# Optimization experiments

Hardware: AMD Instinct MI355X
Metric: run time of the kernel (lower is better)

## Reference

```python
import jax, jax.numpy as jnp
import numpy as np

N = 50000
E = 800000
IN_F = 128
HID = 128
CLS = 32
H = 4
K_HOPS = 2
BETA_MUL = 1.0


def _transconv(x, edge, Wq, bq, Wk, bk, Wv, bv):
    # x: [N, F_in]; edge: [2, E]; W*: [A, F_in]; b*: [A]
    n = x.shape[0]
    q = x @ Wq.T + bq
    k = x @ Wk.T + bk
    v = x @ Wv.T + bv
    A = q.shape[1]
    d_k = A // H
    q = q.reshape(n, H, d_k)
    k = k.reshape(n, H, d_k)
    v = v.reshape(n, H, d_k)
    src, dst = edge[0], edge[1]
    # per-edge dot-product scores: [E, H]
    scores = jnp.einsum('ehd,ehd->eh', q[src], k[dst]) / float(np.sqrt(d_k))
    # segment softmax over source node index (torch_geometric softmax semantics)
    m = jax.ops.segment_max(scores, src, num_segments=n)
    e = jnp.exp(scores - m[src])
    denom = jax.ops.segment_sum(e, src, num_segments=n)
    attn = e / (denom[src] + 1e-16)
    # spmm: out[src] += attn * v[dst], per head; head-major concat == reshape
    msg = attn[:, :, None] * v[dst]              # [E, H, d_k]
    out = jax.ops.segment_sum(msg, src, num_segments=n)  # [N, H, d_k]
    return out.reshape(n, H * d_k)


def _layer(feat, edges, Wq, bq, Wk, bk, Wv, bv):
    # HigherOrderGATLayer with agg_type='sum' + single head with agg_func='mean'
    out = None
    for kk in range(K_HOPS):
        beta = 1.0 if kk == 0 else BETA_MUL / (kk + 1)
        p = beta * _transconv(feat, edges[kk], Wq[kk], bq[kk], Wk[kk], bk[kk], Wv[kk], bv[kk])
        out = p if out is None else out + p
    return out


def setup_inputs() -> dict:
    key = jax.random.key(0)
    ks = jax.random.split(key, 20)
    s = 0.05
    inp = {
        'x': jax.random.normal(ks[0], (N, IN_F), dtype=jnp.float32),
        'Wq0': s * jax.random.normal(ks[1], (K_HOPS, HID, IN_F), dtype=jnp.float32),
        'bq0': s * jax.random.normal(ks[2], (K_HOPS, HID), dtype=jnp.float32),
        'Wk0': s * jax.random.normal(ks[3], (K_HOPS, HID, IN_F), dtype=jnp.float32),
        'bk0': s * jax.random.normal(ks[4], (K_HOPS, HID), dtype=jnp.float32),
        'Wv0': s * jax.random.normal(ks[5], (K_HOPS, HID, IN_F), dtype=jnp.float32),
        'bv0': s * jax.random.normal(ks[6], (K_HOPS, HID), dtype=jnp.float32),
        'Wq1': s * jax.random.normal(ks[7], (K_HOPS, CLS, HID), dtype=jnp.float32),
        'bq1': s * jax.random.normal(ks[8], (K_HOPS, CLS), dtype=jnp.float32),
        'Wk1': s * jax.random.normal(ks[9], (K_HOPS, CLS, HID), dtype=jnp.float32),
        'bk1': s * jax.random.normal(ks[10], (K_HOPS, CLS), dtype=jnp.float32),
        'Wv1': s * jax.random.normal(ks[11], (K_HOPS, CLS, HID), dtype=jnp.float32),
        'bv1': s * jax.random.normal(ks[12], (K_HOPS, CLS), dtype=jnp.float32),
        'edge_l0_k0': jax.random.randint(ks[13], (2, E), 0, N, dtype=jnp.int32).astype(jnp.int64),
        'edge_l0_k1': jax.random.randint(ks[14], (2, E), 0, N, dtype=jnp.int32).astype(jnp.int64),
        'edge_l1_k0': jax.random.randint(ks[15], (2, E), 0, N, dtype=jnp.int32).astype(jnp.int64),
        'edge_l1_k1': jax.random.randint(ks[16], (2, E), 0, N, dtype=jnp.int32).astype(jnp.int64),
    }
    return inp


def reference(x, Wq0, bq0, Wk0, bk0, Wv0, bv0, Wq1, bq1, Wk1, bk1, Wv1, bv1,
              edge_l0_k0, edge_l0_k1, edge_l1_k0, edge_l1_k1):
    edges0 = [edge_l0_k0, edge_l0_k1]
    edges1 = [edge_l1_k0, edge_l1_k1]
    h = jax.nn.elu(_layer(x, edges0, Wq0, bq0, Wk0, bk0, Wv0, bv0))
    logits = _layer(h, edges1, Wq1, bq1, Wk1, bk1, Wv1, bv1)
    return jax.nn.log_softmax(logits, axis=-1)
```

## Files before the change

### kernel.cpp

```cpp
#include <hip/hip_runtime.h>
#include <hip/hip_bf16.h>
#include <math.h>

#define N_NODES 50000
#define N_EDGES 800000
#define IN_F    128
#define HID     128
#define CLS     32
#define NHEAD   4
#define NBUCK   196

typedef __attribute__((ext_vector_type(8))) short  short8;
typedef __attribute__((ext_vector_type(4))) float  floatx4;
typedef __attribute__((ext_vector_type(2))) float  f32x2;
typedef _Float16 h2 __attribute__((ext_vector_type(2)));

static __device__ __forceinline__ unsigned short f2bf(float f) {
    unsigned int u = __float_as_uint(f);
    return (unsigned short)((u + 0x7fffu + ((u >> 16) & 1u)) >> 16);
}
static __device__ __forceinline__ unsigned short f2h(float f) {
    return __builtin_bit_cast(unsigned short, (_Float16)f);
}
static __device__ __forceinline__ h2 uh2(unsigned int u) {
    return __builtin_bit_cast(h2, u);
}
static __device__ __forceinline__ float elu1(float x) {
    return x > 0.f ? x : expm1f(x);
}

static __device__ __forceinline__ float dot8h(uint4 qw, uint4 kw) {
    h2 d = uh2(qw.x) * uh2(kw.x);
    d += uh2(qw.y) * uh2(kw.y);
    d += uh2(qw.z) * uh2(kw.z);
    d += uh2(qw.w) * uh2(kw.w);
    return (float)d.x + (float)d.y;
}

static __device__ __forceinline__ float dot8f8(const float* qf, uint2 kw) {
    f32x2 a0 = __builtin_amdgcn_cvt_pk_f32_fp8((int)kw.x, false);
    f32x2 a1 = __builtin_amdgcn_cvt_pk_f32_fp8((int)kw.x, true);
    f32x2 a2 = __builtin_amdgcn_cvt_pk_f32_fp8((int)kw.y, false);
    f32x2 a3 = __builtin_amdgcn_cvt_pk_f32_fp8((int)kw.y, true);
    return fmaf(qf[0], a0.x, fmaf(qf[1], a0.y, fmaf(qf[2], a1.x, fmaf(qf[3], a1.y,
           fmaf(qf[4], a2.x, fmaf(qf[5], a2.y, fmaf(qf[6], a3.x, qf[7] * a3.y)))))));
}
static __device__ __forceinline__ void acc8f8(float* ax, float e, uint2 vw) {
    f32x2 a0 = __builtin_amdgcn_cvt_pk_f32_fp8((int)vw.x, false);
    f32x2 a1 = __builtin_amdgcn_cvt_pk_f32_fp8((int)vw.x, true);
    f32x2 a2 = __builtin_amdgcn_cvt_pk_f32_fp8((int)vw.y, false);
    f32x2 a3 = __builtin_amdgcn_cvt_pk_f32_fp8((int)vw.y, true);
    ax[0] = fmaf(e, a0.x, ax[0]); ax[1] = fmaf(e, a0.y, ax[1]);
    ax[2] = fmaf(e, a1.x, ax[2]); ax[3] = fmaf(e, a1.y, ax[3]);
    ax[4] = fmaf(e, a2.x, ax[4]); ax[5] = fmaf(e, a2.y, ax[5]);
    ax[6] = fmaf(e, a3.x, ax[6]); ax[7] = fmaf(e, a3.y, ax[7]);
}

__global__ __launch_bounds__(256) void conv6(
    const float* __restrict__ a0, const float* __restrict__ a1, const float* __restrict__ a2,
    const float* __restrict__ a3, const float* __restrict__ a4, const float* __restrict__ a5,
    unsigned short* __restrict__ o0, unsigned short* __restrict__ o1, unsigned short* __restrict__ o2,
    unsigned short* __restrict__ o3, unsigned short* __restrict__ o4, unsigned short* __restrict__ o5,
    int cBig, int cSmall)
{
    const float* srcs[6] = {a0, a1, a2, a3, a4, a5};
    unsigned short* dsts[6] = {o0, o1, o2, o3, o4, o5};
    int s = blockIdx.y;
    int count = (s < 3) ? cBig : cSmall;
    int i = blockIdx.x * 256 + threadIdx.x;
    if (i < count) dsts[s][i] = f2bf(srcs[s][i]);
}

__global__ __launch_bounds__(256) void bucket_hist(
    const int* __restrict__ e0, const int* __restrict__ e1,
    const int* __restrict__ e2, const int* __restrict__ e3,
    int* __restrict__ bcnt, int nE)
{
    const int s = blockIdx.y;
    const int* ep = (s == 0) ? e0 : (s == 1) ? e1 : (s == 2) ? e2 : e3;
    __shared__ int h[NBUCK];
    for (int i = threadIdx.x; i < NBUCK; i += 256) h[i] = 0;
    __syncthreads();
    for (int e = blockIdx.x * 256 + threadIdx.x; e < nE; e += gridDim.x * 256)
        atomicAdd(&h[ep[e] >> 8], 1);
    __syncthreads();
    for (int i = threadIdx.x; i < NBUCK; i += 256)
        if (h[i]) atomicAdd(&bcnt[s * NBUCK + i], h[i]);
}

__global__ __launch_bounds__(256) void bucket_scan(
    const int* __restrict__ bcnt, int* __restrict__ bbase, int* __restrict__ bcur)
{
    int s = blockIdx.x;
    __shared__ int tmp[256];
    int v = (threadIdx.x < NBUCK) ? bcnt[s * NBUCK + threadIdx.x] : 0;
    tmp[threadIdx.x] = v; __syncthreads();
    for (int o = 1; o < 256; o <<= 1) {
        int t = (threadIdx.x >= o) ? tmp[threadIdx.x - o] : 0;
        __syncthreads(); tmp[threadIdx.x] += t; __syncthreads();
    }
    int excl = tmp[threadIdx.x] - v;
    if (threadIdx.x < NBUCK) {
        bbase[s * (NBUCK + 1) + threadIdx.x] = excl;
        bcur[s * NBUCK + threadIdx.x] = excl;
    }
    if (threadIdx.x == NBUCK - 1)
        bbase[s * (NBUCK + 1) + NBUCK] = excl + v;
}

#define TILE 8192
__global__ __launch_bounds__(256) void pass1_scatter(
    const int* __restrict__ e0, const int* __restrict__ e1,
    const int* __restrict__ e2, const int* __restrict__ e3,
    int* __restrict__ bcur, unsigned int* __restrict__ pairs, int nE)
{
    const int s = blockIdx.y;
    const int* ep = (s == 0) ? e0 : (s == 1) ? e1 : (s == 2) ? e2 : e3;
    const int tile0 = blockIdx.x * TILE;
    __shared__ int hist[NBUCK], base[NBUCK], cur[NBUCK];
    for (int i = threadIdx.x; i < NBUCK; i += 256) { hist[i] = 0; cur[i] = 0; }
    __syncthreads();
    for (int i = threadIdx.x; i < TILE; i += 256) {
        int e = tile0 + i;
        if (e < nE) atomicAdd(&hist[ep[e] >> 8], 1);
    }
    __syncthreads();
    for (int i = threadIdx.x; i < NBUCK; i += 256)
        base[i] = hist[i] ? atomicAdd(&bcur[s * NBUCK + i], hist[i]) : 0;
    __syncthreads();
    unsigned int* pp = pairs + (size_t)s * nE;
    for (int i = threadIdx.x; i < TILE; i += 256) {
        int e = tile0 + i;
        if (e < nE) {
            int src = ep[e], dst = ep[e + nE];
            int b = src >> 8;
            int r = atomicAdd(&cur[b], 1);
            pp[base[b] + r] = ((unsigned int)(src & 255) << 16) | (unsigned int)dst;
        }
    }
}

__global__ __launch_bounds__(256) void pass2_place(
    const unsigned int* __restrict__ pairs, const int* __restrict__ bbase,
    int* __restrict__ rowptr, int* __restrict__ deg, int* __restrict__ col,
    int nE, int n)
{
    const int s = blockIdx.y, b = blockIdx.x;
    const int base0 = bbase[s * (NBUCK + 1) + b];
    const int ecnt  = bbase[s * (NBUCK + 1) + b + 1] - base0;
    const unsigned int* pp = pairs + (size_t)s * nE + base0;
    __shared__ int hist[256], cur[256];
    hist[threadIdx.x] = 0;
    __syncthreads();
    for (int i = threadIdx.x; i < ecnt; i += 256)
        atomicAdd(&hist[(pp[i] >> 16) & 255], 1);
    __syncthreads();
    int v = hist[threadIdx.x];
    cur[threadIdx.x] = v; __syncthreads();
    for (int o = 1; o < 256; o <<= 1) {
        int t = (threadIdx.x >= o) ? cur[threadIdx.x - o] : 0;
        __syncthreads(); cur[threadIdx.x] += t; __syncthreads();
    }
    int excl = cur[threadIdx.x] - v;
    int node = b * 256 + threadIdx.x;
    if (node < n) {
        rowptr[(size_t)s * n + node] = base0 + excl;
        deg[(size_t)s * n + node] = v;
    }
    __syncthreads();
    cur[threadIdx.x] = excl;
    __syncthreads();
    int* colp = col + (size_t)s * nE + base0;
    for (int i = threadIdx.x; i < ecnt; i += 256) {
        unsigned int pr = pp[i];
        int r = atomicAdd(&cur[(pr >> 16) & 255], 1);
        colp[r] = (int)(pr & 0xffffu);
    }
}

static __device__ __forceinline__ short8 pack8(const float* p) {
    float4 a = *(const float4*)p;
    float4 b = *(const float4*)(p + 4);
    short8 v;
    v[0] = (short)f2bf(a.x); v[1] = (short)f2bf(a.y);
    v[2] = (short)f2bf(a.z); v[3] = (short)f2bf(a.w);
    v[4] = (short)f2bf(b.x); v[5] = (short)f2bf(b.y);
    v[6] = (short)f2bf(b.z); v[7] = (short)f2bf(b.w);
    return v;
}

template<int A, bool KV8>
__global__ __launch_bounds__(256) void qkv_lds(
    const float* __restrict__ x,
    const unsigned short* __restrict__ Wq, const float* __restrict__ bq,
    const unsigned short* __restrict__ Wk, const float* __restrict__ bk,
    const unsigned short* __restrict__ Wv, const float* __restrict__ bv,
    unsigned short* __restrict__ q0, unsigned short* __restrict__ q1,
    void* __restrict__ k0, void* __restrict__ k1,
    void* __restrict__ v0, void* __restrict__ v1,
    int n)
{
    constexpr int NT   = A / 16;
    constexpr int WROW = IN_F + 8;
    constexpr int OROW = A + 8;
    __shared__ unsigned short Wb[A * WROW];
    __shared__ unsigned short Ob[64 * OROW];

    const int t    = threadIdx.x;
    const int wave = t >> 6;
    const int lane = t & 63;
    const int r    = lane & 15;
    const int kg   = lane >> 4;
    const int node0 = blockIdx.x * 64;
    const int myrow = wave * 16 + r;
    const int xnode = min(node0 + myrow, n - 1);

    short8 xf[4];
    const float* xr = x + (size_t)xnode * IN_F + kg * 8;
#pragma unroll
    for (int ks = 0; ks < 4; ++ks) xf[ks] = pack8(xr + ks * 32);

    const size_t off = (size_t)A * IN_F;
    const unsigned short* Ws[6] = {Wq, Wk, Wv, Wq + off, Wk + off, Wv + off};
    const float*          bs[6] = {bq, bk, bv, bq + A, bk + A, bv + A};
    void*                 os[6] = {q0, k0, v0, q1, k1, v1};

    for (int s = 0; s < 6; ++s) {
        const unsigned short* Wg = Ws[s];
#pragma unroll
        for (int it = 0; it < A * IN_F / 2048; ++it) {
            int e = (it * 256 + t) * 8;
            int row = e / IN_F, c = e % IN_F;
            *(uint4*)&Wb[row * WROW + c] = *(const uint4*)&Wg[e];
        }
        __syncthreads();

        floatx4 acc[NT];
        const float* b = bs[s];
#pragma unroll
        for (int nt = 0; nt < NT; ++nt) {
            float4 b4 = *(const float4*)(b + nt * 16 + kg * 4);
            acc[nt] = (floatx4){b4.x, b4.y, b4.z, b4.w};
        }
#pragma unroll
        for (int ks = 0; ks < 4; ++ks) {
#pragma unroll
            for (int nt = 0; nt < NT; ++nt) {
                short8 wf = *(const short8*)&Wb[(nt * 16 + r) * WROW + ks * 32 + kg * 8];
                acc[nt] = __builtin_amdgcn_mfma_f32_16x16x32_bf16(wf, xf[ks], acc[nt], 0, 0, 0);
            }
        }

        const bool f8 = KV8 && (s != 0) && (s != 3);
        if (f8) {
            unsigned char* Obb = (unsigned char*)Ob;
#pragma unroll
            for (int nt = 0; nt < NT; ++nt) {
                int p = __builtin_amdgcn_cvt_pk_fp8_f32(acc[nt][0], acc[nt][1], 0, false);
                p     = __builtin_amdgcn_cvt_pk_fp8_f32(acc[nt][2], acc[nt][3], p, true);
                *(unsigned int*)&Obb[myrow * OROW + nt * 16 + kg * 4] = (unsigned int)p;
            }
        } else {
#pragma unroll
            for (int nt = 0; nt < NT; ++nt) {
                unsigned int lo = (unsigned int)f2h(acc[nt][0]) | ((unsigned int)f2h(acc[nt][1]) << 16);
                unsigned int hi = (unsigned int)f2h(acc[nt][2]) | ((unsigned int)f2h(acc[nt][3]) << 16);
                *(uint2*)&Ob[myrow * OROW + nt * 16 + kg * 4] = make_uint2(lo, hi);
            }
        }
        __syncthreads();

        if (f8) {
            const unsigned char* Obb = (const unsigned char*)Ob;
            unsigned char* og = (unsigned char*)os[s];
#pragma unroll
            for (int it = 0; it < 64 * A / 2048; ++it) {
                int g = (it * 256 + t) * 8;
                int row = g / A, c = g % A;
                int gn = node0 + row;
                if (gn < n)
                    *(uint2*)&og[(size_t)gn * A + c] = *(const uint2*)&Obb[row * OROW + c];
            }
        } else {
            unsigned short* og = (unsigned short*)os[s];
#pragma unroll
            for (int it = 0; it < 64 * A / 2048; ++it) {
                int g = (it * 256 + t) * 8;
                int row = g / A, c = g % A;
                int gn = node0 + row;
                if (gn < n)
                    *(uint4*)&og[(size_t)gn * A + c] = *(const uint4*)&Ob[row * OROW + c];
            }
        }
        __syncthreads();
    }
}

__device__ __forceinline__ void gat_phase128(
    const unsigned short* __restrict__ q, const uint2* __restrict__ kb,
    const uint2* __restrict__ vb,
    const int* __restrict__ rowptr, const int* __restrict__ deg,
    const int* __restrict__ col,
    int wid, int eslot, int il, float scale, float* r)
{
    uint4 qw = *(const uint4*)(q + (size_t)wid * 128 + il * 8);
    float qf[8];
    {
        h2 t0 = uh2(qw.x), t1 = uh2(qw.y), t2 = uh2(qw.z), t3 = uh2(qw.w);
        qf[0] = (float)t0.x; qf[1] = (float)t0.y;
        qf[2] = (float)t1.x; qf[3] = (float)t1.y;
        qf[4] = (float)t2.x; qf[5] = (float)t2.y;
        qf[6] = (float)t3.x; qf[7] = (float)t3.y;
    }
    int start = rowptr[wid], cnt = deg[wid];
    float l = 0.f;
    float ax[8];
#pragma unroll
    for (int j = 0; j < 8; ++j) ax[j] = 0.f;

    int t = eslot;
    for (; t + 4 < cnt; t += 8) {
        int d0 = col[start + t], d1 = col[start + t + 4];
        uint2 kw0 = kb[(size_t)d0 * 16 + il];
        uint2 kw1 = kb[(size_t)d1 * 16 + il];
        uint2 vw0 = vb[(size_t)d0 * 16 + il];
        uint2 vw1 = vb[(size_t)d1 * 16 + il];
        float p0 = dot8f8(qf, kw0);
        float p1 = dot8f8(qf, kw1);
        p0 += __shfl_xor(p0, 1); p0 += __shfl_xor(p0, 2);
        p1 += __shfl_xor(p1, 1); p1 += __shfl_xor(p1, 2);
        float e0 = __expf(p0 * scale);
        float e1 = __expf(p1 * scale);
        l += e0 + e1;
        acc8f8(ax, e0, vw0);
        acc8f8(ax, e1, vw1);
    }
    for (; t < cnt; t += 4) {
        int d = col[start + t];
        uint2 kw = kb[(size_t)d * 16 + il];
        uint2 vw = vb[(size_t)d * 16 + il];
        float p = dot8f8(qf, kw);
        p += __shfl_xor(p, 1); p += __shfl_xor(p, 2);
        float e = __expf(p * scale);
        l += e;
        acc8f8(ax, e, vw);
    }
#pragma unroll
    for (int off = 16; off <= 32; off <<= 1) {
        l += __shfl_xor(l, off);
#pragma unroll
        for (int j = 0; j < 8; ++j) ax[j] += __shfl_xor(ax[j], off);
    }
    float inv = (l > 0.f) ? 1.f / l : 0.f;
#pragma unroll
    for (int j = 0; j < 8; ++j) r[j] = ax[j] * inv;
}

__global__ __launch_bounds__(256) void gat2_128(
    const unsigned short* __restrict__ q0, const unsigned short* __restrict__ q1,
    const uint2* __restrict__ k0, const uint2* __restrict__ v0,
    const uint2* __restrict__ k1, const uint2* __restrict__ v1,
    const int* __restrict__ rp0, const int* __restrict__ dg0, const int* __restrict__ cl0,
    const int* __restrict__ rp1, const int* __restrict__ dg1, const int* __restrict__ cl1,
    float* __restrict__ out, float scale, int n)
{
    int wid  = (blockIdx.x * 256 + threadIdx.x) >> 6;
    int lane = threadIdx.x & 63;
    if (wid >= n) return;
    int eslot = lane >> 4, il = lane & 15;

    float r0[8], r1[8];
    gat_phase128(q0, k0, v0, rp0, dg0, cl0, wid, eslot, il, scale, r0);
    gat_phase128(q1, k1, v1, rp1, dg1, cl1, wid, eslot, il, scale, r1);

    if (eslot == 0) {
        float z[8];
#pragma unroll
        for (int j = 0; j < 8; ++j) z[j] = elu1(r0[j] + 0.5f * r1[j]);
        float4* op = (float4*)(out + (size_t)wid * 128 + il * 8);
        op[0] = make_float4(z[0], z[1], z[2], z[3]);
        op[1] = make_float4(z[4], z[5], z[6], z[7]);
    }
}

__device__ __forceinline__ void gat_phase32(
    const unsigned short* __restrict__ q, const uint4* __restrict__ kb,
    const uint4* __restrict__ vb,
    const int* __restrict__ rowptr, const int* __restrict__ deg,
    const int* __restrict__ col,
    int wid, int eslot, int il, float scale, float* r)
{
    uint4 qw = *(const uint4*)(q + (size_t)wid * 32 + il * 8);
    int start = rowptr[wid], cnt = deg[wid];
    float l = 0.f;
    h2 ax2[4];
#pragma unroll
    for (int j = 0; j < 4; ++j) ax2[j] = (h2){(_Float16)0.f, (_Float16)0.f};

    for (int t = eslot; t < cnt; t += 16) {
        int d = col[start + t];
        uint4 kw = kb[(size_t)d * 4 + il];
        uint4 vw = vb[(size_t)d * 4 + il];
        float p = dot8h(qw, kw);
        float e = __expf(p * scale);
        l += e;
        _Float16 h = (_Float16)e;
        h2 e2 = (h2){h, h};
        ax2[0] += e2 * uh2(vw.x); ax2[1] += e2 * uh2(vw.y);
        ax2[2] += e2 * uh2(vw.z); ax2[3] += e2 * uh2(vw.w);
    }
    float ax[8];
#pragma unroll
    for (int j = 0; j < 4; ++j) { ax[2 * j] = (float)ax2[j].x; ax[2 * j + 1] = (float)ax2[j].y; }
#pragma unroll
    for (int off = 4; off <= 32; off <<= 1) {
        l += __shfl_xor(l, off);
#pragma unroll
        for (int j = 0; j < 8; ++j) ax[j] += __shfl_xor(ax[j], off);
    }
    float inv = (l > 0.f) ? 1.f / l : 0.f;
#pragma unroll
    for (int j = 0; j < 8; ++j) r[j] = ax[j] * inv;
}

__global__ __launch_bounds__(256) void gat2_32(
    const unsigned short* __restrict__ q0, const unsigned short* __restrict__ q1,
    const uint4* __restrict__ k0, const uint4* __restrict__ v0,
    const uint4* __restrict__ k1, const uint4* __restrict__ v1,
    const int* __restrict__ rp0, const int* __restrict__ dg0, const int* __restrict__ cl0,
    const int* __restrict__ rp1, const int* __restrict__ dg1, const int* __restrict__ cl1,
    float* __restrict__ outp, float scale, int n)
{
    int wid  = (blockIdx.x * 256 + threadIdx.x) >> 6;
    int lane = threadIdx.x & 63;
    if (wid >= n) return;
    int eslot = lane >> 2, il = lane & 3;

    float r0[8], r1[8];
    gat_phase32(q0, k0, v0, rp0, dg0, cl0, wid, eslot, il, scale, r0);
    gat_phase32(q1, k1, v1, rp1, dg1, cl1, wid, eslot, il, scale, r1);

    if (eslot == 0) {
        float z[8];
#pragma unroll
        for (int j = 0; j < 8; ++j) z[j] = r0[j] + 0.5f * r1[j];
        float mx = z[0];
#pragma unroll
        for (int j = 1; j < 8; ++j) mx = fmaxf(mx, z[j]);
        mx = fmaxf(mx, __shfl_xor(mx, 1));
        mx = fmaxf(mx, __shfl_xor(mx, 2));
        float sm = 0.f;
#pragma unroll
        for (int j = 0; j < 8; ++j) sm += __expf(z[j] - mx);
        sm += __shfl_xor(sm, 1);
        sm += __shfl_xor(sm, 2);
        float lse = mx + logf(sm);
        float4* op = (float4*)(outp + (size_t)wid * 32 + il * 8);
        op[0] = make_float4(z[0] - lse, z[1] - lse, z[2] - lse, z[3] - lse);
        op[1] = make_float4(z[4] - lse, z[5] - lse, z[6] - lse, z[7] - lse);
    }
}

extern "C" void kernel_launch(void* const* d_in, const int* in_sizes, int n_in,
                              void* d_out, int out_size, void* d_ws, size_t ws_size,
                              hipStream_t stream)
{
    const float* x   = (const float*)d_in[0];
    const float* Wq0 = (const float*)d_in[1];
    const float* bq0 = (const float*)d_in[2];
    const float* Wk0 = (const float*)d_in[3];
    const float* bk0 = (const float*)d_in[4];
    const float* Wv0 = (const float*)d_in[5];
    const float* bv0 = (const float*)d_in[6];
    const float* Wq1 = (const float*)d_in[7];
    const float* bq1 = (const float*)d_in[8];
    const float* Wk1 = (const float*)d_in[9];
    const float* bk1 = (const float*)d_in[10];
    const float* Wv1 = (const float*)d_in[11];
    const float* bv1 = (const float*)d_in[12];
    const int* e0 = (const int*)d_in[13];
    const int* e1 = (const int*)d_in[14];
    const int* e2 = (const int*)d_in[15];
    const int* e3 = (const int*)d_in[16];

    char* w = (char*)d_ws;
    unsigned short* q0h = (unsigned short*)w; w += (size_t)N_NODES * HID * 2;
    unsigned short* q1h = (unsigned short*)w; w += (size_t)N_NODES * HID * 2;
    unsigned char*  k0c = (unsigned char*)w;  w += (size_t)N_NODES * HID;
    unsigned char*  v0c = (unsigned char*)w;  w += (size_t)N_NODES * HID;
    unsigned char*  k1c = (unsigned char*)w;  w += (size_t)N_NODES * HID;
    unsigned char*  v1c = (unsigned char*)w;  w += (size_t)N_NODES * HID;
    float*          acc = (float*)w;          w += (size_t)N_NODES * HID * 4;
    int* deg    = (int*)w; w += (size_t)4 * N_NODES * 4;
    int* rowptr = (int*)w; w += (size_t)4 * N_NODES * 4;
    int* col    = (int*)w; w += (size_t)4 * N_EDGES * 4;
    int* bcnt   = (int*)w; w += (size_t)4 * NBUCK * 4;
    int* bbase  = (int*)w; w += (size_t)4 * (NBUCK + 1) * 4;
    int* bcur   = (int*)w; w += (size_t)4 * NBUCK * 4;
    unsigned short* wq0b = (unsigned short*)w; w += (size_t)2 * HID * IN_F * 2;
    unsigned short* wk0b = (unsigned short*)w; w += (size_t)2 * HID * IN_F * 2;
    unsigned short* wv0b = (unsigned short*)w; w += (size_t)2 * HID * IN_F * 2;
    unsigned short* wq1b = (unsigned short*)w; w += (size_t)2 * CLS * IN_F * 2;
    unsigned short* wk1b = (unsigned short*)w; w += (size_t)2 * CLS * IN_F * 2;
    unsigned short* wv1b = (unsigned short*)w; w += (size_t)2 * CLS * IN_F * 2;

    unsigned int* pairs = (unsigned int*)q0h;
    unsigned short* qA0 = q0h;
    unsigned short* qA1 = q0h + (size_t)N_NODES * CLS;
    unsigned short* kA0 = q0h + (size_t)2 * N_NODES * CLS;
    unsigned short* vA0 = q0h + (size_t)3 * N_NODES * CLS;
    unsigned short* kA1 = q1h;
    unsigned short* vA1 = q1h + (size_t)N_NODES * CLS;

    float* out = (float*)d_out;
    const int NB = (N_NODES + 3) / 4;
    const int QB = (N_NODES + 63) / 64;
    const float sc0 = 1.f / sqrtf(32.f), sc1 = 1.f / sqrtf(8.f);

    const int W0 = 2 * HID * IN_F, W1 = 2 * CLS * IN_F;
    conv6<<<dim3((W0 + 255) / 256, 6), 256, 0, stream>>>(
        Wq0, Wk0, Wv0, Wq1, Wk1, Wv1, wq0b, wk0b, wv0b, wq1b, wk1b, wv1b, W0, W1);

    hipMemsetAsync(bcnt, 0, (size_t)4 * NBUCK * 4, stream);
    bucket_hist<<<dim3(256, 4), 256, 0, stream>>>(e0, e1, e2, e3, bcnt, N_EDGES);
    bucket_scan<<<4, 256, 0, stream>>>(bcnt, bbase, bcur);
    pass1_scatter<<<dim3((N_EDGES + TILE - 1) / TILE, 4), 256, 0, stream>>>(
        e0, e1, e2, e3, bcur, pairs, N_EDGES);
    pass2_place<<<dim3(NBUCK, 4), 256, 0, stream>>>(
        pairs, bbase, rowptr, deg, col, N_EDGES, N_NODES);

    qkv_lds<HID, true><<<QB, 256, 0, stream>>>(
        x, wq0b, bq0, wk0b, bk0, wv0b, bv0,
        q0h, q1h, k0c, k1c, v0c, v1c, N_NODES);
    gat2_128<<<NB, 256, 0, stream>>>(
        q0h, q1h,
        (const uint2*)k0c, (const uint2*)v0c, (const uint2*)k1c, (const uint2*)v1c,
        rowptr,            deg,            col,
        rowptr + N_NODES,  deg + N_NODES,  col + N_EDGES,
        acc, sc0, N_NODES);

    qkv_lds<CLS, false><<<QB, 256, 0, stream>>>(
        acc, wq1b, bq1, wk1b, bk1, wv1b, bv1,
        qA0, qA1, kA0, kA1, vA0, vA1, N_NODES);
    gat2_32<<<NB, 256, 0, stream>>>(
        qA0, qA1,
        (const uint4*)kA0, (const uint4*)vA0, (const uint4*)kA1, (const uint4*)vA1,
        rowptr + 2 * N_NODES, deg + 2 * N_NODES, col + (size_t)2 * N_EDGES,
        rowptr + 3 * N_NODES, deg + 3 * N_NODES, col + (size_t)3 * N_EDGES,
        out, sc1, N_NODES);
}
```

Baseline: 283.9 us.

## Store layer-1 keys and values in FP8 and use 32-bit gather indexing

After: 281.1 us. No clear change (-1.0%).

```diff
diff --git a/kernel.cpp b/kernel.cpp
--- a/kernel.cpp
+++ b/kernel.cpp
@@ -29,21 +29,16 @@
     return x > 0.f ? x : expm1f(x);
 }
 
-static __device__ __forceinline__ float dot8h(uint4 qw, uint4 kw) {
-    h2 d = uh2(qw.x) * uh2(kw.x);
-    d += uh2(qw.y) * uh2(kw.y);
-    d += uh2(qw.z) * uh2(kw.z);
-    d += uh2(qw.w) * uh2(kw.w);
-    return (float)d.x + (float)d.y;
-}
-
 static __device__ __forceinline__ float dot8f8(const float* qf, uint2 kw) {
     f32x2 a0 = __builtin_amdgcn_cvt_pk_f32_fp8((int)kw.x, false);
     f32x2 a1 = __builtin_amdgcn_cvt_pk_f32_fp8((int)kw.x, true);
     f32x2 a2 = __builtin_amdgcn_cvt_pk_f32_fp8((int)kw.y, false);
     f32x2 a3 = __builtin_amdgcn_cvt_pk_f32_fp8((int)kw.y, true);
-    return fmaf(qf[0], a0.x, fmaf(qf[1], a0.y, fmaf(qf[2], a1.x, fmaf(qf[3], a1.y,
-           fmaf(qf[4], a2.x, fmaf(qf[5], a2.y, fmaf(qf[6], a3.x, qf[7] * a3.y)))))));
+    float p0 = fmaf(qf[0], a0.x, qf[1] * a0.y);
+    p0 = fmaf(qf[2], a1.x, fmaf(qf[3], a1.y, p0));
+    float p1 = fmaf(qf[4], a2.x, qf[5] * a2.y);
+    p1 = fmaf(qf[6], a3.x, fmaf(qf[7], a3.y, p1));
+    return p0 + p1;
 }
 static __device__ __forceinline__ void acc8f8(float* ax, float e, uint2 vw) {
     f32x2 a0 = __builtin_amdgcn_cvt_pk_f32_fp8((int)vw.x, false);
@@ -216,7 +211,7 @@
     const int xnode = min(node0 + myrow, n - 1);
 
     short8 xf[4];
-    const float* xr = x + (size_t)xnode * IN_F + kg * 8;
+    const float* xr = x + (unsigned)xnode * IN_F + kg * 8;
 #pragma unroll
     for (int ks = 0; ks < 4; ++ks) xf[ks] = pack8(xr + ks * 32);
 
@@ -279,7 +274,7 @@
                 int row = g / A, c = g % A;
                 int gn = node0 + row;
                 if (gn < n)
-                    *(uint2*)&og[(size_t)gn * A + c] = *(const uint2*)&Obb[row * OROW + c];
+                    *(uint2*)&og[(unsigned)gn * A + c] = *(const uint2*)&Obb[row * OROW + c];
             }
         } else {
             unsigned short* og = (unsigned short*)os[s];
@@ -289,7 +284,7 @@
                 int row = g / A, c = g % A;
                 int gn = node0 + row;
                 if (gn < n)
-                    *(uint4*)&og[(size_t)gn * A + c] = *(const uint4*)&Ob[row * OROW + c];
+                    *(uint4*)&og[(unsigned)gn * A + c] = *(const uint4*)&Ob[row * OROW + c];
             }
         }
         __syncthreads();
@@ -303,7 +298,7 @@
     const int* __restrict__ col,
     int wid, int eslot, int il, float scale, float* r)
 {
-    uint4 qw = *(const uint4*)(q + (size_t)wid * 128 + il * 8);
+    uint4 qw = *(const uint4*)(q + (unsigned)wid * 128u + (unsigned)(il * 8));
     float qf[8];
     {
         h2 t0 = uh2(qw.x), t1 = uh2(qw.y), t2 = uh2(qw.z), t3 = uh2(qw.w);
@@ -320,11 +315,12 @@
 
     int t = eslot;
     for (; t + 4 < cnt; t += 8) {
-        int d0 = col[start + t], d1 = col[start + t + 4];
-        uint2 kw0 = kb[(size_t)d0 * 16 + il];
-        uint2 kw1 = kb[(size_t)d1 * 16 + il];
-        uint2 vw0 = vb[(size_t)d0 * 16 + il];
-        uint2 vw1 = vb[(size_t)d1 * 16 + il];
+        unsigned d0 = (unsigned)col[start + t] * 16u + (unsigned)il;
+        unsigned d1 = (unsigned)col[start + t + 4] * 16u + (unsigned)il;
+        uint2 kw0 = kb[d0];
+        uint2 kw1 = kb[d1];
+        uint2 vw0 = vb[d0];
+        uint2 vw1 = vb[d1];
         float p0 = dot8f8(qf, kw0);
         float p1 = dot8f8(qf, kw1);
         p0 += __shfl_xor(p0, 1); p0 += __shfl_xor(p0, 2);
@@ -336,9 +332,9 @@
         acc8f8(ax, e1, vw1);
     }
     for (; t < cnt; t += 4) {
-        int d = col[start + t];
-        uint2 kw = kb[(size_t)d * 16 + il];
-        uint2 vw = vb[(size_t)d * 16 + il];
+        unsigned d = (unsigned)col[start + t] * 16u + (unsigned)il;
+        uint2 kw = kb[d];
+        uint2 vw = vb[d];
         float p = dot8f8(qf, kw);
         p += __shfl_xor(p, 1); p += __shfl_xor(p, 2);
         float e = __expf(p * scale);
@@ -377,41 +373,43 @@
         float z[8];
 #pragma unroll
         for (int j = 0; j < 8; ++j) z[j] = elu1(r0[j] + 0.5f * r1[j]);
-        float4* op = (float4*)(out + (size_t)wid * 128 + il * 8);
+        float4* op = (float4*)(out + (unsigned)wid * 128u + (unsigned)(il * 8));
         op[0] = make_float4(z[0], z[1], z[2], z[3]);
         op[1] = make_float4(z[4], z[5], z[6], z[7]);
     }
 }
 
 __device__ __forceinline__ void gat_phase32(
-    const unsigned short* __restrict__ q, const uint4* __restrict__ kb,
-    const uint4* __restrict__ vb,
+    const unsigned short* __restrict__ q, const uint2* __restrict__ kb,
+    const uint2* __restrict__ vb,
     const int* __restrict__ rowptr, const int* __restrict__ deg,
     const int* __restrict__ col,
     int wid, int eslot, int il, float scale, float* r)
 {
-    uint4 qw = *(const uint4*)(q + (size_t)wid * 32 + il * 8);
+    uint4 qw = *(const uint4*)(q + (unsigned)wid * 32u + (unsigned)(il * 8));
+    float qf[8];
+    {
+        h2 t0 = uh2(qw.x), t1 = uh2(qw.y), t2 = uh2(qw.z), t3 = uh2(qw.w);
+        qf[0] = (float)t0.x; qf[1] = (float)t0.y;
+        qf[2] = (float)t1.x; qf[3] = (float)t1.y;
+        qf[4] = (float)t2.x; qf[5] = (float)t2.y;
+        qf[6] = (float)t3.x; qf[7] = (float)t3.y;
+    }
     int start = rowptr[wid], cnt = deg[wid];
     float l = 0.f;
-    h2 ax2[4];
-#pragma unroll
-    for (int j = 0; j < 4; ++j) ax2[j] = (h2){(_Float16)0.f, (_Float16)0.f};
+    float ax[8];
+#pragma unroll
+    for (int j = 0; j < 8; ++j) ax[j] = 0.f;
 
     for (int t = eslot; t < cnt; t += 16) {
-        int d = col[start + t];
-        uint4 kw = kb[(size_t)d * 4 + il];
-        uint4 vw = vb[(size_t)d * 4 + il];
-        float p = dot8h(qw, kw);
+        unsigned d = (unsigned)col[start + t] * 4u + (unsigned)il;
+        uint2 kw = kb[d];
+        uint2 vw = vb[d];
+        float p = dot8f8(qf, kw);
         float e = __expf(p * scale);
         l += e;
-        _Float16 h = (_Float16)e;
-        h2 e2 = (h2){h, h};
-        ax2[0] += e2 * uh2(vw.x); ax2[1] += e2 * uh2(vw.y);
-        ax2[2] += e2 * uh2(vw.z); ax2[3] += e2 * uh2(vw.w);
-    }
-    float ax[8];
-#pragma unroll
-    for (int j = 0; j < 4; ++j) { ax[2 * j] = (float)ax2[j].x; ax[2 * j + 1] = (float)ax2[j].y; }
+        acc8f8(ax, e, vw);
+    }
 #pragma unroll
     for (int off = 4; off <= 32; off <<= 1) {
         l += __shfl_xor(l, off);
@@ -425,8 +423,8 @@
 
 __global__ __launch_bounds__(256) void gat2_32(
     const unsigned short* __restrict__ q0, const unsigned short* __restrict__ q1,
-    const uint4* __restrict__ k0, const uint4* __restrict__ v0,
-    const uint4* __restrict__ k1, const uint4* __restrict__ v1,
+    const uint2* __restrict__ k0, const uint2* __restrict__ v0,
+    const uint2* __restrict__ k1, const uint2* __restrict__ v1,
     const int* __restrict__ rp0, const int* __restrict__ dg0, const int* __restrict__ cl0,
     const int* __restrict__ rp1, const int* __restrict__ dg1, const int* __restrict__ cl1,
     float* __restrict__ outp, float scale, int n)
@@ -455,7 +453,7 @@
         sm += __shfl_xor(sm, 1);
         sm += __shfl_xor(sm, 2);
         float lse = mx + logf(sm);
-        float4* op = (float4*)(outp + (size_t)wid * 32 + il * 8);
+        float4* op = (float4*)(outp + (unsigned)wid * 32u + (unsigned)(il * 8));
         op[0] = make_float4(z[0] - lse, z[1] - lse, z[2] - lse, z[3] - lse);
         op[1] = make_float4(z[4] - lse, z[5] - lse, z[6] - lse, z[7] - lse);
     }
@@ -507,10 +505,10 @@
     unsigned int* pairs = (unsigned int*)q0h;
     unsigned short* qA0 = q0h;
     unsigned short* qA1 = q0h + (size_t)N_NODES * CLS;
-    unsigned short* kA0 = q0h + (size_t)2 * N_NODES * CLS;
-    unsigned short* vA0 = q0h + (size_t)3 * N_NODES * CLS;
-    unsigned short* kA1 = q1h;
-    unsigned short* vA1 = q1h + (size_t)N_NODES * CLS;
+    unsigned char*  kA0 = (unsigned char*)(q0h + (size_t)2 * N_NODES * CLS);
+    unsigned char*  vA0 = kA0 + (size_t)N_NODES * CLS;
+    unsigned char*  kA1 = (unsigned char*)q1h;
+    unsigned char*  vA1 = kA1 + (size_t)N_NODES * CLS;
 
     float* out = (float*)d_out;
     const int NB = (N_NODES + 3) / 4;
@@ -539,12 +537,12 @@
         rowptr + N_NODES,  deg + N_NODES,  col + N_EDGES,
         acc, sc0, N_NODES);
 
-    qkv_lds<CLS, false><<<QB, 256, 0, stream>>>(
+    qkv_lds<CLS, true><<<QB, 256, 0, stream>>>(
         acc, wq1b, bq1, wk1b, bk1, wv1b, bv1,
         qA0, qA1, kA0, kA1, vA0, vA1, N_NODES);
     gat2_32<<<NB, 256, 0, stream>>>(
         qA0, qA1,
-        (const uint4*)kA0, (const uint4*)vA0, (const uint4*)kA1, (const uint4*)vA1,
+        (const uint2*)kA0, (const uint2*)vA0, (const uint2*)kA1, (const uint2*)vA1,
         rowptr + 2 * N_NODES, deg + 2 * N_NODES, col + (size_t)2 * N_EDGES,
         rowptr + 3 * N_NODES, deg + 3 * N_NODES, col + (size_t)3 * N_EDGES,
         out, sc1, N_NODES);
```
